# Performance work log

Measured on AMD Instinct MI355X. Metric: run time of the kernel, lower is better.

## Reference

```python
import jax, jax.numpy as jnp
import numpy as np

N = 8192


def setup_inputs() -> dict:
    key = jax.random.key(0)
    ks = jax.random.split(key, 12)
    H_emb = jax.random.normal(ks[0], (645, 1140), jnp.float32) * 0.05
    H_emb = H_emb.at[0].set(0.0)  # padding_idx=0
    inp = {
        "ld_gcn": jax.random.normal(ks[1], (N, 512), jnp.float32),
        "ld_encoder": jax.random.normal(ks[2], (N, 512), jnp.float32),
        "x": jax.random.randint(ks[3], (N,), 0, 240),
        "y": jax.random.randint(ks[4], (N,), 0, 404),
        "H_emb": H_emb,
        "conv_w": jax.random.normal(ks[5], (32, 1, 2, 25), jnp.float32) * (1.0 / np.sqrt(2 * 25)),
        "conv_b": jnp.zeros((32,), jnp.float32),
        "W1": jax.random.normal(ks[6], (1000, 3968), jnp.float32) * (1.0 / np.sqrt(3968)),
        "b1": jnp.zeros((1000,), jnp.float32),
        "W2": jax.random.normal(ks[7], (100, 1000), jnp.float32) * (1.0 / np.sqrt(1000)),
        "b2": jnp.zeros((100,), jnp.float32),
        "Wg": jax.random.normal(ks[8], (100, 512), jnp.float32) * (1.0 / np.sqrt(512)),
        "bg": jnp.zeros((100,), jnp.float32),
        "We": jax.random.normal(ks[9], (100, 512), jnp.float32) * (1.0 / np.sqrt(512)),
        "be": jnp.zeros((100,), jnp.float32),
    }
    return inp


def reference(ld_gcn, ld_encoder, x, y, H_emb, conv_w, conv_b, W1, b1, W2, b2, Wg, bg, We, be):
    n = x.shape[0]
    lrelu = lambda t: jax.nn.leaky_relu(t, 0.01)
    # embedding lookups + concat -> (n,1,2,1140)
    h = jnp.concatenate([H_emb[x], H_emb[y + 240]], axis=1).reshape(n, 1, 2, 1140)
    # CNN: conv (2,25) stride (1,9) valid -> (n,32,1,124)
    c = jax.lax.conv_general_dilated(h, conv_w, window_strides=(1, 9), padding="VALID",
                                     dimension_numbers=("NCHW", "OIHW", "NCHW"))
    c = lrelu(c + conv_b[None, :, None, None]).reshape(n, -1)  # (n,3968)
    # fc_H (dropout = identity at eval)
    hfc = lrelu(c @ W1.T + b1)
    hfc = lrelu(hfc @ W2.T + b2)  # (n,100)
    # gating projections
    g = jnp.tanh(ld_gcn @ Wg.T + bg)       # (n,100)
    e = jnp.tanh(ld_encoder @ We.T + be)   # (n,100)
    # diagonal of (n,100)@(100,n) == row-wise dot product
    a_gcn = jnp.einsum("nd,nd->n", g, hfc)
    a_enc = jnp.einsum("nd,nd->n", e, hfc)
    att = jax.nn.softmax(jnp.stack([a_gcn, a_enc], axis=1), axis=1)  # (n,2)
    return ld_gcn * att[:, :1], ld_encoder * att[:, 1:]
```

## Files before the change

### kernel.cpp

```cpp
#include <hip/hip_runtime.h>
#include <hip/hip_bf16.h>

typedef unsigned short u16;
typedef short bf16x8 __attribute__((ext_vector_type(8)));
typedef float f32x4 __attribute__((ext_vector_type(4)));

#define NROWS 8192
#define EMBD  1140
#define FDIM  3968
#define N1R   1000
#define N1P   1024
#define N2R   100
#define N2P   128
#define DG    512

__device__ inline u16 f2b(float f) {
  __hip_bfloat16 h = __float2bfloat16(f);
  return *reinterpret_cast<u16*>(&h);
}

__device__ inline float tanh_fast(float x) {
  float ax = fabsf(x);
  float t = __expf(-2.f * ax);
  float r = (1.f - t) / (1.f + t);
  return x < 0.f ? -r : r;
}

__device__ inline void gld16(const void* g, void* l) {
  __builtin_amdgcn_global_load_lds(
      (const __attribute__((address_space(1))) unsigned int*)g,
      (__attribute__((address_space(3))) unsigned int*)l, 16, 0, 0);
}

__global__ void cvt_pad2_kernel(const float* __restrict__ in, u16* __restrict__ out,
                                int realN, int realK, int NP, int KP) {
  long total = (long)NP * KP;
  long stride = (long)gridDim.x * blockDim.x;
  for (long i = (long)blockIdx.x * blockDim.x + threadIdx.x; i < total; i += stride) {
    int n = (int)(i / KP);
    int k = (int)(i - (long)n * KP);
    float v = (n < realN && k < realK) ? in[(long)n * realK + k] : 0.f;
    out[i] = f2b(v);
  }
}

__global__ __launch_bounds__(256) void precomp_ab_kernel(
    const float* __restrict__ H_emb, const float* __restrict__ conv_w,
    const float* __restrict__ conv_b, float* __restrict__ Abuf, float* __restrict__ Bbuf) {
  int b = blockIdx.x;
  bool isA = b < 240;
  const float* emb = H_emb + (size_t)b * EMBD;
  float* outp = isA ? (Abuf + (size_t)b * FDIM) : (Bbuf + (size_t)(b - 240) * FDIM);
  __shared__ float se[EMBD];
  __shared__ float sw[32 * 25];
  __shared__ float sb[32];
  int t = threadIdx.x;
  for (int i = t; i < EMBD; i += 256) se[i] = emb[i];
  int kh = isA ? 0 : 1;
  for (int i = t; i < 800; i += 256) {
    int o = i / 25, kw = i - o * 25;
    sw[i] = conv_w[o * 50 + kh * 25 + kw];
  }
  if (t < 32) sb[t] = isA ? conv_b[t] : 0.f;
  __syncthreads();
  for (int f = t; f < FDIM; f += 256) {
    int o = f / 124, wpos = f - o * 124;
    const float* e = se + wpos * 9;
    const float* wp = sw + o * 25;
    float acc = sb[o];
#pragma unroll
    for (int kw = 0; kw < 25; ++kw) acc += wp[kw] * e[kw];
    outp[f] = acc;
  }
}

__global__ __launch_bounds__(256) void conv_combine_kernel(
    const float* __restrict__ Abuf, const float* __restrict__ Bbuf,
    const int* __restrict__ xi, const int* __restrict__ yi, u16* __restrict__ cbf) {
  int r = blockIdx.x;
  const float4* pa = (const float4*)(Abuf + (size_t)xi[r] * FDIM);
  const float4* pb = (const float4*)(Bbuf + (size_t)yi[r] * FDIM);
  u16* out = cbf + (size_t)r * FDIM;
  for (int i = threadIdx.x; i < FDIM / 4; i += 256) {
    float4 a = pa[i], b = pb[i];
    float v0 = a.x + b.x, v1 = a.y + b.y, v2 = a.z + b.z, v3 = a.w + b.w;
    v0 = v0 > 0.f ? v0 : 0.01f * v0;
    v1 = v1 > 0.f ? v1 : 0.01f * v1;
    v2 = v2 > 0.f ? v2 : 0.01f * v2;
    v3 = v3 > 0.f ? v3 : 0.01f * v3;
    ushort4 o;
    o.x = f2b(v0); o.y = f2b(v1); o.z = f2b(v2); o.w = f2b(v3);
    *(ushort4*)(out + i * 4) = o;
  }
}

__global__ __launch_bounds__(256) void fc1_kernel(
    const u16* __restrict__ A, const u16* __restrict__ B,
    const float* __restrict__ bias, int realN,
    u16* __restrict__ C, int K, int ldc, int nTilesX) {
  const int nwg = gridDim.x;
  const int cpx = nwg >> 3;
  const int bid = blockIdx.x;
  const int wg = (bid & 7) * cpx + (bid >> 3);
  const int tm = (wg / nTilesX) * 128;
  const int tn = (wg % nTilesX) * 128;

  __shared__ u16 As[128 * 32];
  __shared__ u16 Bs[128 * 32];
  const int t = threadIdx.x;
  const int lane = t & 63;
  const int w = t >> 6;
  const int wr = (w >> 1) * 64, wc = (w & 1) * 64;
  const int fr = lane & 15;
  const int kg = lane >> 4;

  const int grow = w * 16 + (lane >> 2);
  const int gcol = (lane & 3) * 8;
  const u16* gA0 = A + (size_t)(tm + grow) * K + gcol;
  const u16* gA1 = A + (size_t)(tm + grow + 64) * K + gcol;
  const u16* gB0 = B + (size_t)(tn + grow) * K + gcol;
  const u16* gB1 = B + (size_t)(tn + grow + 64) * K + gcol;
  u16* lA0 = As + w * 512;
  u16* lA1 = lA0 + 4 * 512;
  u16* lB0 = Bs + w * 512;
  u16* lB1 = lB0 + 4 * 512;

  f32x4 acc[4][4];
#pragma unroll
  for (int m = 0; m < 4; ++m)
#pragma unroll
    for (int n = 0; n < 4; ++n) acc[m][n] = (f32x4){0.f, 0.f, 0.f, 0.f};

  const int nk = K >> 5;
  for (int kt = 0; kt < nk; ++kt) {
    __syncthreads();
    const int ko = kt * 32;
    gld16(gA0 + ko, lA0);
    gld16(gA1 + ko, lA1);
    gld16(gB0 + ko, lB0);
    gld16(gB1 + ko, lB1);
    __syncthreads();
    bf16x8 af[4], bff[4];
#pragma unroll
    for (int m = 0; m < 4; ++m)
      af[m] = *(const bf16x8*)(As + (wr + m * 16 + fr) * 32 + kg * 8);
#pragma unroll
    for (int n = 0; n < 4; ++n)
      bff[n] = *(const bf16x8*)(Bs + (wc + n * 16 + fr) * 32 + kg * 8);
#pragma unroll
    for (int m = 0; m < 4; ++m)
#pragma unroll
      for (int n = 0; n < 4; ++n)
        acc[m][n] = __builtin_amdgcn_mfma_f32_16x16x32_bf16(af[m], bff[n], acc[m][n], 0, 0, 0);
  }

#pragma unroll
  for (int n = 0; n < 4; ++n) {
    int col = tn + wc + n * 16 + fr;
    float bv = (col < realN) ? bias[col] : 0.f;
#pragma unroll
    for (int m = 0; m < 4; ++m) {
#pragma unroll
      for (int j = 0; j < 4; ++j) {
        int row = tm + wr + m * 16 + kg * 4 + j;
        float v = acc[m][n][j] + bv;
        v = v > 0.f ? v : 0.01f * v;
        C[(size_t)row * ldc + col] = f2b(v);
      }
    }
  }
}

__global__ __launch_bounds__(256) void tail_kernel(
    const u16* __restrict__ hfc1, const u16* __restrict__ W2bf, const float* __restrict__ b2,
    const float* __restrict__ ldg, const float* __restrict__ lde,
    const u16* __restrict__ Wgbf, const float* __restrict__ bg,
    const u16* __restrict__ Webf, const float* __restrict__ be,
    float* __restrict__ out0, float* __restrict__ out1) {
  __shared__ float H16[N2P][16];
  __shared__ float dpart[2][4][16];
  __shared__ float wt[2][16];

  const int tm = blockIdx.x * 16;
  const int t = threadIdx.x;
  const int lane = t & 63;
  const int w = t >> 6;
  const int fr = lane & 15;
  const int kg = lane >> 4;
  const int n0 = w * 2;

  {
    f32x4 a0 = (f32x4){0.f, 0.f, 0.f, 0.f}, a1 = a0;
    const u16* Ap = hfc1 + (size_t)(tm + fr) * N1P + kg * 8;
    const u16* B0 = W2bf + (size_t)(n0 * 16 + fr) * N1P + kg * 8;
    const u16* B1 = B0 + (size_t)16 * N1P;
#pragma unroll 8
    for (int kt = 0; kt < N1P / 32; ++kt) {
      bf16x8 af = *(const bf16x8*)(Ap + kt * 32);
      bf16x8 f0 = *(const bf16x8*)(B0 + kt * 32);
      bf16x8 f1 = *(const bf16x8*)(B1 + kt * 32);
      a0 = __builtin_amdgcn_mfma_f32_16x16x32_bf16(af, f0, a0, 0, 0, 0);
      a1 = __builtin_amdgcn_mfma_f32_16x16x32_bf16(af, f1, a1, 0, 0, 0);
    }
#pragma unroll
    for (int n = 0; n < 2; ++n) {
      int col = (n0 + n) * 16 + fr;
      float bv = (col < N2R) ? b2[col] : 0.f;
      f32x4 v = n == 0 ? a0 : a1;
      f32x4 o;
#pragma unroll
      for (int j = 0; j < 4; ++j) {
        float x = v[j] + bv;
        o[j] = x > 0.f ? x : 0.01f * x;
      }
      *(f32x4*)&H16[col][kg * 4] = o;
    }
  }
  __syncthreads();

#pragma unroll 1
  for (int sec = 0; sec < 2; ++sec) {
    const float* ld = sec == 0 ? ldg : lde;
    const u16* Wb = sec == 0 ? Wgbf : Webf;
    const float* bb = sec == 0 ? bg : be;

    f32x4 a0 = (f32x4){0.f, 0.f, 0.f, 0.f}, a1 = a0;
    const float* Ap = ld + (size_t)(tm + fr) * DG + kg * 8;
    const u16* B0 = Wb + (size_t)(n0 * 16 + fr) * DG + kg * 8;
    const u16* B1 = B0 + (size_t)16 * DG;
#pragma unroll 4
    for (int kt = 0; kt < DG / 32; ++kt) {
      float4 v0 = *(const float4*)(Ap + kt * 32);
      float4 v1 = *(const float4*)(Ap + kt * 32 + 4);
      bf16x8 af;
      af[0] = (short)f2b(v0.x); af[1] = (short)f2b(v0.y);
      af[2] = (short)f2b(v0.z); af[3] = (short)f2b(v0.w);
      af[4] = (short)f2b(v1.x); af[5] = (short)f2b(v1.y);
      af[6] = (short)f2b(v1.z); af[7] = (short)f2b(v1.w);
      bf16x8 f0 = *(const bf16x8*)(B0 + kt * 32);
      bf16x8 f1 = *(const bf16x8*)(B1 + kt * 32);
      a0 = __builtin_amdgcn_mfma_f32_16x16x32_bf16(af, f0, a0, 0, 0, 0);
      a1 = __builtin_amdgcn_mfma_f32_16x16x32_bf16(af, f1, a1, 0, 0, 0);
    }
    float dv[4] = {0.f, 0.f, 0.f, 0.f};
#pragma unroll
    for (int n = 0; n < 2; ++n) {
      int col = (n0 + n) * 16 + fr;
      float bv = (col < N2R) ? bb[col] : 0.f;
      f32x4 v = n == 0 ? a0 : a1;
      f32x4 h = *(const f32x4*)&H16[col][kg * 4];
#pragma unroll
      for (int j = 0; j < 4; ++j)
        dv[j] += tanh_fast(v[j] + bv) * h[j];
    }
#pragma unroll
    for (int j = 0; j < 4; ++j) {
      float v = dv[j];
      v += __shfl_xor(v, 1);
      v += __shfl_xor(v, 2);
      v += __shfl_xor(v, 4);
      v += __shfl_xor(v, 8);
      dv[j] = v;
    }
    if (fr == 0) {
#pragma unroll
      for (int j = 0; j < 4; ++j) dpart[sec][w][kg * 4 + j] = dv[j];
    }
  }
  __syncthreads();

  if (t < 16) {
    float ag = dpart[0][0][t] + dpart[0][1][t] + dpart[0][2][t] + dpart[0][3][t];
    float ae = dpart[1][0][t] + dpart[1][1][t] + dpart[1][2][t] + dpart[1][3][t];
    float mm = fmaxf(ag, ae);
    float eg = __expf(ag - mm), eo = __expf(ae - mm);
    float inv = 1.f / (eg + eo);
    wt[0][t] = eg * inv;
    wt[1][t] = eo * inv;
  }
  __syncthreads();

  for (int i = t; i < 16 * (DG / 4); i += 256) {
    int r = i >> 7, c = i & 127;
    float w0 = wt[0][r], w1 = wt[1][r];
    size_t off = (size_t)(tm + r) * DG + c * 4;
    float4 a = *(const float4*)(ldg + off);
    a.x *= w0; a.y *= w0; a.z *= w0; a.w *= w0;
    *(float4*)(out0 + off) = a;
    float4 b = *(const float4*)(lde + off);
    b.x *= w1; b.y *= w1; b.z *= w1; b.w *= w1;
    *(float4*)(out1 + off) = b;
  }
}

extern "C" void kernel_launch(void* const* d_in, const int* in_sizes, int n_in,
                              void* d_out, int out_size, void* d_ws, size_t ws_size,
                              hipStream_t stream) {
  const float* ld_gcn = (const float*)d_in[0];
  const float* ld_enc = (const float*)d_in[1];
  const int*   xi     = (const int*)d_in[2];
  const int*   yi     = (const int*)d_in[3];
  const float* H_emb  = (const float*)d_in[4];
  const float* conv_w = (const float*)d_in[5];
  const float* conv_b = (const float*)d_in[6];
  const float* W1     = (const float*)d_in[7];
  const float* b1     = (const float*)d_in[8];
  const float* W2     = (const float*)d_in[9];
  const float* b2     = (const float*)d_in[10];
  const float* Wg     = (const float*)d_in[11];
  const float* bg     = (const float*)d_in[12];
  const float* We     = (const float*)d_in[13];
  const float* be     = (const float*)d_in[14];

  char* ws = (char*)d_ws;
  size_t off = 0;
  auto alloc = [&](size_t bytes) -> void* {
    void* p = ws + off;
    off = (off + bytes + 255) & ~(size_t)255;
    return p;
  };
  float* Abuf = (float*)alloc(240ull * FDIM * 4);
  float* Bbuf = (float*)alloc(404ull * FDIM * 4);
  u16*   cbf  = (u16*)  alloc((size_t)NROWS * FDIM * 2);
  u16*   W1bf = (u16*)  alloc((size_t)N1P * FDIM * 2);
  u16*   W2bf = (u16*)  alloc((size_t)N2P * N1P * 2);
  u16*   Wgbf = (u16*)  alloc((size_t)N2P * DG * 2);
  u16*   Webf = (u16*)  alloc((size_t)N2P * DG * 2);
  u16*   hfc1 = (u16*)  alloc((size_t)NROWS * N1P * 2);
  if (ws_size < off) return;

  cvt_pad2_kernel<<<4096, 256, 0, stream>>>(W1, W1bf, N1R, FDIM, N1P, FDIM);
  cvt_pad2_kernel<<<512, 256, 0, stream>>>(W2, W2bf, N2R, N1R, N2P, N1P);
  cvt_pad2_kernel<<<256, 256, 0, stream>>>(Wg, Wgbf, N2R, DG, N2P, DG);
  cvt_pad2_kernel<<<256, 256, 0, stream>>>(We, Webf, N2R, DG, N2P, DG);
  precomp_ab_kernel<<<644, 256, 0, stream>>>(H_emb, conv_w, conv_b, Abuf, Bbuf);
  conv_combine_kernel<<<NROWS, 256, 0, stream>>>(Abuf, Bbuf, xi, yi, cbf);

  fc1_kernel<<<dim3((NROWS / 128) * (N1P / 128)), 256, 0, stream>>>(
      cbf, W1bf, b1, N1R, hfc1, FDIM, N1P, N1P / 128);

  float* out0 = (float*)d_out;
  float* out1 = out0 + (size_t)NROWS * DG;
  tail_kernel<<<NROWS / 16, 256, 0, stream>>>(
      hfc1, W2bf, b2, ld_gcn, ld_enc, Wgbf, bg, Webf, be, out0, out1);
}
```

Before: 219.8 us.

## Double-buffer fc1 GEMM with K=64 swizzled LDS tiles and fuse prep kernels

The fc1 GEMM now uses two LDS buffers with a K-step of 64 and an XOR-swizzled layout, so the next tile is prefetched while MFMAs run on the current one, with one barrier per step instead of two. The four weight-conversion launches and the conv precompute are merged into a single prep kernel that converts eight elements per thread, which cuts launch overhead and widens memory accesses. LDS per block rises to 64KB, which may lower occupancy.

Measured after the change: 196.6 us. 10.6% less time.

```diff
diff --git a/kernel.cpp b/kernel.cpp
--- a/kernel.cpp
+++ b/kernel.cpp
@@ -32,29 +32,60 @@
       (__attribute__((address_space(3))) unsigned int*)l, 16, 0, 0);
 }
 
-__global__ void cvt_pad2_kernel(const float* __restrict__ in, u16* __restrict__ out,
-                                int realN, int realK, int NP, int KP) {
-  long total = (long)NP * KP;
-  long stride = (long)gridDim.x * blockDim.x;
-  for (long i = (long)blockIdx.x * blockDim.x + threadIdx.x; i < total; i += stride) {
-    int n = (int)(i / KP);
-    int k = (int)(i - (long)n * KP);
-    float v = (n < realN && k < realK) ? in[(long)n * realK + k] : 0.f;
-    out[i] = f2b(v);
-  }
-}
-
-__global__ __launch_bounds__(256) void precomp_ab_kernel(
+__global__ __launch_bounds__(256) void prep_kernel(
+    const float* __restrict__ W1, const float* __restrict__ W2,
+    const float* __restrict__ Wg, const float* __restrict__ We,
     const float* __restrict__ H_emb, const float* __restrict__ conv_w,
-    const float* __restrict__ conv_b, float* __restrict__ Abuf, float* __restrict__ Bbuf) {
-  int b = blockIdx.x;
-  bool isA = b < 240;
-  const float* emb = H_emb + (size_t)b * EMBD;
-  float* outp = isA ? (Abuf + (size_t)b * FDIM) : (Bbuf + (size_t)(b - 240) * FDIM);
+    const float* __restrict__ conv_b,
+    u16* __restrict__ W1bf, u16* __restrict__ W2bf,
+    u16* __restrict__ Wgbf, u16* __restrict__ Webf,
+    float* __restrict__ Abuf, float* __restrict__ Bbuf) {
+  const int b = blockIdx.x;
+  const int t = threadIdx.x;
+  if (b < 2112) {
+    const float* src;
+    u16* dst;
+    int row, c8, realRow, realCol;
+    if (b < 1984) {
+      int id = b * 256 + t;
+      row = id / 496; c8 = (id - row * 496) * 8;
+      src = W1 + (size_t)row * FDIM + c8;
+      dst = W1bf + (size_t)row * FDIM + c8;
+      realRow = N1R; realCol = FDIM;
+    } else if (b < 2048) {
+      int id = (b - 1984) * 256 + t;
+      row = id >> 7; c8 = (id & 127) * 8;
+      src = W2 + (size_t)row * N1R + c8;
+      dst = W2bf + (size_t)row * N1P + c8;
+      realRow = N2R; realCol = N1R;
+    } else if (b < 2080) {
+      int id = (b - 2048) * 256 + t;
+      row = id >> 6; c8 = (id & 63) * 8;
+      src = Wg + (size_t)row * DG + c8;
+      dst = Wgbf + (size_t)row * DG + c8;
+      realRow = N2R; realCol = DG;
+    } else {
+      int id = (b - 2080) * 256 + t;
+      row = id >> 6; c8 = (id & 63) * 8;
+      src = We + (size_t)row * DG + c8;
+      dst = Webf + (size_t)row * DG + c8;
+      realRow = N2R; realCol = DG;
+    }
+    bf16x8 o = (bf16x8){0, 0, 0, 0, 0, 0, 0, 0};
+    if (row < realRow && c8 < realCol) {
+#pragma unroll
+      for (int j = 0; j < 8; ++j) o[j] = (short)f2b(src[j]);
+    }
+    *(bf16x8*)dst = o;
+    return;
+  }
   __shared__ float se[EMBD];
   __shared__ float sw[32 * 25];
   __shared__ float sb[32];
-  int t = threadIdx.x;
+  const int eb = b - 2112;
+  bool isA = eb < 240;
+  const float* emb = H_emb + (size_t)eb * EMBD;
+  float* outp = isA ? (Abuf + (size_t)eb * FDIM) : (Bbuf + (size_t)(eb - 240) * FDIM);
   for (int i = t; i < EMBD; i += 256) se[i] = emb[i];
   int kh = isA ? 0 : 1;
   for (int i = t; i < 800; i += 256) {
@@ -105,8 +136,8 @@
   const int tm = (wg / nTilesX) * 128;
   const int tn = (wg % nTilesX) * 128;
 
-  __shared__ u16 As[128 * 32];
-  __shared__ u16 Bs[128 * 32];
+  __shared__ u16 As[2][8192];
+  __shared__ u16 Bs[2][8192];
   const int t = threadIdx.x;
   const int lane = t & 63;
   const int w = t >> 6;
@@ -114,16 +145,18 @@
   const int fr = lane & 15;
   const int kg = lane >> 4;
 
-  const int grow = w * 16 + (lane >> 2);
-  const int gcol = (lane & 3) * 8;
-  const u16* gA0 = A + (size_t)(tm + grow) * K + gcol;
-  const u16* gA1 = A + (size_t)(tm + grow + 64) * K + gcol;
-  const u16* gB0 = B + (size_t)(tn + grow) * K + gcol;
-  const u16* gB1 = B + (size_t)(tn + grow + 64) * K + gcol;
-  u16* lA0 = As + w * 512;
-  u16* lA1 = lA0 + 4 * 512;
-  u16* lB0 = Bs + w * 512;
-  u16* lB1 = lB0 + 4 * 512;
+  const int srow = lane >> 3;
+  const int su = ((lane & 7) ^ srow) * 8;
+  const u16* gA[4];
+  const u16* gB[4];
+  int ldsOff[4];
+#pragma unroll
+  for (int i = 0; i < 4; ++i) {
+    const int c = w + i * 4;
+    gA[i] = A + (size_t)(tm + c * 8 + srow) * K + su;
+    gB[i] = B + (size_t)(tn + c * 8 + srow) * K + su;
+    ldsOff[i] = c * 512;
+  }
 
   f32x4 acc[4][4];
 #pragma unroll
@@ -131,27 +164,42 @@
 #pragma unroll
     for (int n = 0; n < 4; ++n) acc[m][n] = (f32x4){0.f, 0.f, 0.f, 0.f};
 
-  const int nk = K >> 5;
+  const int nk = K >> 6;
+#pragma unroll
+  for (int i = 0; i < 4; ++i) {
+    gld16(gA[i], &As[0][ldsOff[i]]);
+    gld16(gB[i], &Bs[0][ldsOff[i]]);
+  }
+  __syncthreads();
+
   for (int kt = 0; kt < nk; ++kt) {
+    const int cb = kt & 1;
+    if (kt + 1 < nk) {
+      const int ko = (kt + 1) << 6;
+#pragma unroll
+      for (int i = 0; i < 4; ++i) {
+        gld16(gA[i] + ko, &As[cb ^ 1][ldsOff[i]]);
+        gld16(gB[i] + ko, &Bs[cb ^ 1][ldsOff[i]]);
+      }
+    }
+    __builtin_amdgcn_sched_barrier(0);
+#pragma unroll
+    for (int ks = 0; ks < 2; ++ks) {
+      const int un = ((ks * 4 + kg) ^ (fr & 7)) << 4;
+      bf16x8 af[4], bff[4];
+#pragma unroll
+      for (int m = 0; m < 4; ++m)
+        af[m] = *(const bf16x8*)((const char*)As[cb] + (wr + m * 16 + fr) * 128 + un);
+#pragma unroll
+      for (int n = 0; n < 4; ++n)
+        bff[n] = *(const bf16x8*)((const char*)Bs[cb] + (wc + n * 16 + fr) * 128 + un);
+#pragma unroll
+      for (int m = 0; m < 4; ++m)
+#pragma unroll
+        for (int n = 0; n < 4; ++n)
+          acc[m][n] = __builtin_amdgcn_mfma_f32_16x16x32_bf16(af[m], bff[n], acc[m][n], 0, 0, 0);
+    }
     __syncthreads();
-    const int ko = kt * 32;
-    gld16(gA0 + ko, lA0);
-    gld16(gA1 + ko, lA1);
-    gld16(gB0 + ko, lB0);
-    gld16(gB1 + ko, lB1);
-    __syncthreads();
-    bf16x8 af[4], bff[4];
-#pragma unroll
-    for (int m = 0; m < 4; ++m)
-      af[m] = *(const bf16x8*)(As + (wr + m * 16 + fr) * 32 + kg * 8);
-#pragma unroll
-    for (int n = 0; n < 4; ++n)
-      bff[n] = *(const bf16x8*)(Bs + (wc + n * 16 + fr) * 32 + kg * 8);
-#pragma unroll
-    for (int m = 0; m < 4; ++m)
-#pragma unroll
-      for (int n = 0; n < 4; ++n)
-        acc[m][n] = __builtin_amdgcn_mfma_f32_16x16x32_bf16(af[m], bff[n], acc[m][n], 0, 0, 0);
   }
 
 #pragma unroll
@@ -329,11 +377,8 @@
   u16*   hfc1 = (u16*)  alloc((size_t)NROWS * N1P * 2);
   if (ws_size < off) return;
 
-  cvt_pad2_kernel<<<4096, 256, 0, stream>>>(W1, W1bf, N1R, FDIM, N1P, FDIM);
-  cvt_pad2_kernel<<<512, 256, 0, stream>>>(W2, W2bf, N2R, N1R, N2P, N1P);
-  cvt_pad2_kernel<<<256, 256, 0, stream>>>(Wg, Wgbf, N2R, DG, N2P, DG);
-  cvt_pad2_kernel<<<256, 256, 0, stream>>>(We, Webf, N2R, DG, N2P, DG);
-  precomp_ab_kernel<<<644, 256, 0, stream>>>(H_emb, conv_w, conv_b, Abuf, Bbuf);
+  prep_kernel<<<2756, 256, 0, stream>>>(W1, W2, Wg, We, H_emb, conv_w, conv_b,
+                                        W1bf, W2bf, Wgbf, Webf, Abuf, Bbuf);
   conv_combine_kernel<<<NROWS, 256, 0, stream>>>(Abuf, Bbuf, xi, yi, cbf);
 
   fc1_kernel<<<dim3((NROWS / 128) * (N1P / 128)), 256, 0, stream>>>(
```
